# Performance work log

Hardware: AMD Instinct MI355X
Metric: run time of the kernel (lower is better)

## Reference

```python
import jax, jax.numpy as jnp
import numpy as np

TOP_K = 2

def setup_inputs() -> dict:
    key = jax.random.key(0)
    ks = jax.random.split(key, 8)
    B, S, H, E, F = 4, 2048, 1024, 8, 2048  # F = hidden * expansion(2)
    scale_in = 0.02
    return {
        "x": jax.random.normal(ks[0], (B, S, H), dtype=jnp.float32),
        "router_w": jax.random.normal(ks[1], (H, E), dtype=jnp.float32) * scale_in,
        "router_b": jnp.zeros((E,), dtype=jnp.float32),
        "w1": jax.random.normal(ks[2], (E, H, F), dtype=jnp.float32) * scale_in,
        "b1": jnp.zeros((E, F), dtype=jnp.float32),
        "w2": jax.random.normal(ks[3], (E, F, H), dtype=jnp.float32) * scale_in,
        "b2": jnp.zeros((E, H), dtype=jnp.float32),
    }

def reference(x, router_w, router_b, w1, b1, w2, b2):
    B, S, H = x.shape
    E = router_b.shape[0]
    T = B * S
    flat = x.reshape(T, H)
    # Router + top-k gating (softmax over the k selected logits, as in torch code)
    logits = flat @ router_w + router_b                       # [T, E]
    topk_scores, topk_idx = jax.lax.top_k(logits, TOP_K)      # [T, k]
    probs = jax.nn.softmax(topk_scores, axis=-1)              # [T, k]
    # Dense gate matrix: gates[t, e] = prob if e selected for token t else 0
    gates = jnp.zeros((T, E), dtype=flat.dtype).at[
        jnp.arange(T)[:, None], topk_idx
    ].add(probs)                                              # [T, E]
    # Expert FFNs computed as batched GEMMs over the expert axis
    h = jax.nn.relu(jnp.einsum('td,edf->etf', flat, w1) + b1[:, None, :])  # [E, T, F]
    eout = jnp.einsum('etf,efd->etd', h, w2) + b2[:, None, :]              # [E, T, H]
    out = jnp.einsum('etd,te->td', eout, gates)                            # [T, H]
    return out.reshape(B, S, H)
```

## Files before the change

### kernel.cpp

```cpp
#include <hip/hip_runtime.h>
#include <hip/hip_bf16.h>

#define T_TOK 8192
#define HDIM 1024
#define FDIM 2048
#define NEXP 8
#define NASSIGN (T_TOK * 2)
#define ROWCAP (NASSIGN + 128)
#define NHB 64

typedef __bf16 bf16;
typedef __bf16 bf16x4 __attribute__((ext_vector_type(4)));
typedef __bf16 bf16x8 __attribute__((ext_vector_type(8)));
typedef float f32x4 __attribute__((ext_vector_type(4)));

__device__ __forceinline__ void gload_lds16(const void* g, void* l) {
    __builtin_amdgcn_global_load_lds(
        (const __attribute__((address_space(1))) void*)(uintptr_t)g,
        (__attribute__((address_space(3))) void*)(uintptr_t)l,
        16, 0, 0);
}

__global__ __launch_bounds__(256) void transpose_to_bf16(
    const float* __restrict__ in, bf16* __restrict__ out, int R, int C) {
    __shared__ float tile[64][68];
    int e = blockIdx.z;
    const float* inp = in + (size_t)e * R * C;
    bf16* outp = out + (size_t)e * R * C;
    int c0 = blockIdx.x * 64, r0 = blockIdx.y * 64;
    int tid = threadIdx.x;
    int tx = tid & 15, ty = tid >> 4;
#pragma unroll
    for (int i = 0; i < 4; i++) {
        int row = ty + i * 16;
        float4 v = *(const float4*)&inp[(size_t)(r0 + row) * C + c0 + tx * 4];
        *(float4*)&tile[row][tx * 4] = v;
    }
    __syncthreads();
#pragma unroll
    for (int i = 0; i < 2; i++) {
        int idx = tid + i * 256;
        int c = idx >> 3, seg = idx & 7;
        bf16x8 v;
#pragma unroll
        for (int j = 0; j < 8; j++) v[j] = (bf16)tile[seg * 8 + j][c];
        *(bf16x8*)&outp[(size_t)(c0 + c) * R + r0 + seg * 8] = v;
    }
}

__global__ __launch_bounds__(256) void router_kernel(
    const float* __restrict__ x, const float* __restrict__ rw,
    const float* __restrict__ rb, int* __restrict__ expert_pair,
    float2* __restrict__ gate_pair) {
    __shared__ float rwT[NEXP][HDIM];
    __shared__ float rbs[NEXP];
    int tid = threadIdx.x;
    for (int i = tid; i < HDIM * NEXP / 4; i += 256) {
        float4 v = ((const float4*)rw)[i];
        int h = i >> 1, e0 = (i & 1) * 4;
        rwT[e0 + 0][h] = v.x;
        rwT[e0 + 1][h] = v.y;
        rwT[e0 + 2][h] = v.z;
        rwT[e0 + 3][h] = v.w;
    }
    if (tid < NEXP) rbs[tid] = rb[tid];
    __syncthreads();
    int wave = tid >> 6, lane = tid & 63;
    int tbase = blockIdx.x * 32 + wave * 8;

    for (int tk = 0; tk < 8; tk++) {
        int t = tbase + tk;
        const float4* xt = (const float4*)(x + (size_t)t * HDIM);
        float p[NEXP];
#pragma unroll
        for (int e = 0; e < NEXP; e++) p[e] = 0.f;
#pragma unroll
        for (int it = 0; it < 4; it++) {
            float4 v = xt[it * 64 + lane];
            int h = (it * 64 + lane) * 4;
#pragma unroll
            for (int e = 0; e < NEXP; e++) {
                float4 wv = *(const float4*)&rwT[e][h];
                p[e] += v.x * wv.x + v.y * wv.y + v.z * wv.z + v.w * wv.w;
            }
        }
#pragma unroll
        for (int off = 32; off >= 1; off >>= 1) {
#pragma unroll
            for (int e = 0; e < NEXP; e++) p[e] += __shfl_xor(p[e], off, 64);
        }
        if (lane == 0) {
            float lg[NEXP];
#pragma unroll
            for (int e = 0; e < NEXP; e++) lg[e] = p[e] + rbs[e];
            int e0 = 0;
#pragma unroll
            for (int e = 1; e < NEXP; e++)
                if (lg[e] > lg[e0]) e0 = e;
            int e1 = -1;
#pragma unroll
            for (int e = 0; e < NEXP; e++) {
                if (e == e0) continue;
                if (e1 < 0 || lg[e] > lg[e1]) e1 = e;
            }
            float z = expf(lg[e1] - lg[e0]);
            expert_pair[t] = e0 | (e1 << 16);
            gate_pair[t] = make_float2(1.f / (1.f + z), z / (1.f + z));
        }
    }
}

__global__ __launch_bounds__(256) void hist_kernel(
    const int* __restrict__ expert_pair, int* __restrict__ hist) {
    int tid = threadIdx.x;
    int wave = tid >> 6, lane = tid & 63;
    int a = blockIdx.x * 256 + tid;
    int t = a >> 1, j = a & 1;
    int e = (expert_pair[t] >> (16 * j)) & 0xffff;
    __shared__ int wcnt[4][NEXP];
#pragma unroll
    for (int ee = 0; ee < NEXP; ee++) {
        unsigned long long m = __ballot(e == ee);
        if (lane == 0) wcnt[wave][ee] = __popcll(m);
    }
    __syncthreads();
    if (tid < NEXP)
        hist[blockIdx.x * NEXP + tid] =
            wcnt[0][tid] + wcnt[1][tid] + wcnt[2][tid] + wcnt[3][tid];
}

__global__ __launch_bounds__(256) void scan_kernel(
    const int* __restrict__ hist, int* __restrict__ start,
    int* __restrict__ cnt, int* __restrict__ offs) {
    __shared__ int h[NHB * NEXP];
    __shared__ int tot[NEXP];
    __shared__ int offsh[NEXP];
    int tid = threadIdx.x;
    for (int i = tid; i < NHB * NEXP; i += 256) h[i] = hist[i];
    __syncthreads();
    if (tid < NEXP) {
        int s = 0;
        for (int b = 0; b < NHB; b++) s += h[b * NEXP + tid];
        tot[tid] = s;
        cnt[tid] = s;
    }
    __syncthreads();
    if (tid == 0) {
        int o = 0;
        for (int e = 0; e < NEXP; e++) {
            offsh[e] = o;
            offs[e] = o;
            o += tot[e];
        }
    }
    __syncthreads();
    if (tid < NEXP) {
        int run = offsh[tid];
        for (int b = 0; b < NHB; b++) {
            start[b * NEXP + tid] = run;
            run += h[b * NEXP + tid];
        }
    }
}

__global__ __launch_bounds__(256) void scatter_kernel(
    const int* __restrict__ expert_pair, const float2* __restrict__ gate_pair,
    const int* __restrict__ start, int* __restrict__ perm,
    float* __restrict__ gatebuf, int* __restrict__ rowbuf) {
    int tid = threadIdx.x;
    int wave = tid >> 6, lane = tid & 63;
    int a = blockIdx.x * 256 + tid;
    int t = a >> 1, j = a & 1;
    int e = (expert_pair[t] >> (16 * j)) & 0xffff;
    float2 gp = gate_pair[t];
    float g = j ? gp.y : gp.x;
    __shared__ int wcnt[4][NEXP];
    int rankw = 0;
    unsigned long long below = (1ull << lane) - 1ull;
#pragma unroll
    for (int ee = 0; ee < NEXP; ee++) {
        unsigned long long m = __ballot(e == ee);
        if (lane == 0) wcnt[wave][ee] = __popcll(m);
        if (ee == e) rankw = __popcll(m & below);
    }
    __syncthreads();
    int cross = 0;
    for (int w = 0; w < wave; w++) cross += wcnt[w][e];
    int pos = start[blockIdx.x * NEXP + e] + cross + rankw;
    perm[pos] = t;
    gatebuf[pos] = g;
    rowbuf[a] = pos;
}

__global__ __launch_bounds__(256) void pack_kernel(
    const float* __restrict__ x, const int* __restrict__ perm,
    bf16* __restrict__ xg) {
    int r0 = blockIdx.x * 16;
    int wave = threadIdx.x >> 6, lane = threadIdx.x & 63;
#pragma unroll
    for (int i = 0; i < 4; i++) {
        int row = r0 + wave * 4 + i;
        int tok = perm[row];
        const float* src = x + (size_t)tok * HDIM;
        bf16* dst = xg + (size_t)row * HDIM;
#pragma unroll
        for (int it = 0; it < 4; it++) {
            int c = (it * 64 + lane) * 4;
            float4 v = *(const float4*)&src[c];
            bf16x4 b = {(bf16)v.x, (bf16)v.y, (bf16)v.z, (bf16)v.w};
            *(bf16x4*)&dst[c] = b;
        }
    }
}

template <bool RELU, bool GATE>
__global__ __launch_bounds__(256) void moe_gemm(
    const bf16* __restrict__ A, const bf16* __restrict__ B,
    const float* __restrict__ bias, const float* __restrict__ gates,
    bf16* __restrict__ out, const int* __restrict__ cnt,
    const int* __restrict__ offs, int K, int N) {
    int e = blockIdx.z;
    int n_cnt = cnt[e];
    int m0 = blockIdx.y * 128;
    if (m0 >= n_cnt) return;
    int n0 = blockIdx.x * 128;

    __shared__ bf16 As[128 * 32];
    __shared__ bf16 Bs[128 * 32];

    int tid = threadIdx.x;
    int lane = tid & 63;
    int wave = tid >> 6;
    int wm = (wave & 1) * 64, wn = (wave >> 1) * 64;
    int quad = lane >> 4;
    int l16 = lane & 15;

    int off_e = offs[e];
    const bf16* Ae = A + (size_t)off_e * K;
    const bf16* Be = B + (size_t)e * N * K;

    int srow = lane >> 2;
    int scol = (lane & 3) ^ ((lane >> 2) & 3) ^ ((lane >> 4) & 3);
    const bf16* ag0 = Ae + (size_t)(m0 + wave * 16 + srow) * K + scol * 8;
    const bf16* ag1 = ag0 + (size_t)64 * K;
    const bf16* bg0 = Be + (size_t)(n0 + wave * 16 + srow) * K + scol * 8;
    const bf16* bg1 = bg0 + (size_t)64 * K;
    bf16* as0 = &As[(wave * 16) * 32];
    bf16* as1 = &As[(64 + wave * 16) * 32];
    bf16* bs0 = &Bs[(wave * 16) * 32];
    bf16* bs1 = &Bs[(64 + wave * 16) * 32];

    int dswz = (quad ^ (l16 & 3) ^ ((l16 >> 2) & 3)) * 8;

    f32x4 acc[4][4];
#pragma unroll
    for (int i = 0; i < 4; i++)
#pragma unroll
        for (int j = 0; j < 4; j++) acc[i][j] = f32x4{0.f, 0.f, 0.f, 0.f};

    for (int k0 = 0; k0 < K; k0 += 32) {
        gload_lds16(ag0 + k0, as0);
        gload_lds16(ag1 + k0, as1);
        gload_lds16(bg0 + k0, bs0);
        gload_lds16(bg1 + k0, bs1);
        __syncthreads();
        bf16x8 af[4], bfr[4];
#pragma unroll
        for (int i = 0; i < 4; i++)
            af[i] = *(const bf16x8*)&As[(wm + i * 16 + l16) * 32 + dswz];
#pragma unroll
        for (int j = 0; j < 4; j++)
            bfr[j] = *(const bf16x8*)&Bs[(wn + j * 16 + l16) * 32 + dswz];
#pragma unroll
        for (int i = 0; i < 4; i++)
#pragma unroll
            for (int j = 0; j < 4; j++)
                acc[i][j] = __builtin_amdgcn_mfma_f32_16x16x32_bf16(af[i], bfr[j], acc[i][j], 0, 0, 0);
        __syncthreads();
    }

#pragma unroll
    for (int i = 0; i < 4; i++)
#pragma unroll
        for (int j = 0; j < 4; j++)
#pragma unroll
            for (int r = 0; r < 4; r++) {
                int m = m0 + wm + i * 16 + quad * 4 + r;
                if (m < n_cnt) {
                    int n = n0 + wn + j * 16 + l16;
                    float v = acc[i][j][r] + bias[e * N + n];
                    if (RELU) v = v > 0.f ? v : 0.f;
                    if (GATE) v *= gates[off_e + m];
                    out[(size_t)(off_e + m) * N + n] = (bf16)v;
                }
            }
}

__global__ __launch_bounds__(256) void combine_kernel(
    const bf16* __restrict__ eout, const int* __restrict__ rowbuf,
    float* __restrict__ out) {
    int t = blockIdx.x;
    int r0 = rowbuf[2 * t], r1 = rowbuf[2 * t + 1];
    const bf16* p0 = eout + (size_t)r0 * HDIM;
    const bf16* p1 = eout + (size_t)r1 * HDIM;
    float* o = out + (size_t)t * HDIM;
    int n = threadIdx.x * 4;
    bf16x4 a = *(const bf16x4*)&p0[n];
    bf16x4 b = *(const bf16x4*)&p1[n];
    float4 v = {(float)a[0] + (float)b[0], (float)a[1] + (float)b[1],
                (float)a[2] + (float)b[2], (float)a[3] + (float)b[3]};
    *(float4*)&o[n] = v;
}

extern "C" void kernel_launch(void* const* d_in, const int* in_sizes, int n_in,
                              void* d_out, int out_size, void* d_ws, size_t ws_size,
                              hipStream_t stream) {
    const float* x = (const float*)d_in[0];
    const float* rw = (const float*)d_in[1];
    const float* rb = (const float*)d_in[2];
    const float* w1 = (const float*)d_in[3];
    const float* b1 = (const float*)d_in[4];
    const float* w2 = (const float*)d_in[5];
    const float* b2 = (const float*)d_in[6];
    float* out = (float*)d_out;

    char* ws = (char*)d_ws;
    size_t o = 0;
    auto alloc = [&](size_t bytes) {
        char* p = ws + o;
        o += (bytes + 255) & ~(size_t)255;
        return p;
    };
    bf16* w1t = (bf16*)alloc((size_t)NEXP * FDIM * HDIM * 2);
    bf16* w2t = (bf16*)alloc((size_t)NEXP * HDIM * FDIM * 2);
    bf16* hbuf = (bf16*)alloc((size_t)ROWCAP * FDIM * 2);
    bf16* xg = (bf16*)alloc((size_t)ROWCAP * HDIM * 2);
    bf16* eout = xg;
    int* expert_pair = (int*)alloc((size_t)T_TOK * 4);
    float2* gate_pair = (float2*)alloc((size_t)T_TOK * 8);
    int* hist = (int*)alloc((size_t)NHB * NEXP * 4);
    int* start = (int*)alloc((size_t)NHB * NEXP * 4);
    int* perm = (int*)alloc((size_t)NASSIGN * 4);
    float* gatebuf = (float*)alloc((size_t)NASSIGN * 4);
    int* rowbuf = (int*)alloc((size_t)NASSIGN * 4);
    int* cnt = (int*)alloc(256);
    int* offs = (int*)alloc(256);

    transpose_to_bf16<<<dim3(FDIM / 64, HDIM / 64, NEXP), 256, 0, stream>>>(w1, w1t, HDIM, FDIM);
    transpose_to_bf16<<<dim3(HDIM / 64, FDIM / 64, NEXP), 256, 0, stream>>>(w2, w2t, FDIM, HDIM);
    router_kernel<<<T_TOK / 32, 256, 0, stream>>>(x, rw, rb, expert_pair, gate_pair);
    hist_kernel<<<NHB, 256, 0, stream>>>(expert_pair, hist);
    scan_kernel<<<1, 256, 0, stream>>>(hist, start, cnt, offs);
    scatter_kernel<<<NHB, 256, 0, stream>>>(expert_pair, gate_pair, start, perm, gatebuf, rowbuf);
    pack_kernel<<<NASSIGN / 16, 256, 0, stream>>>(x, perm, xg);
    moe_gemm<true, false><<<dim3(FDIM / 128, T_TOK / 128, NEXP), 256, 0, stream>>>(
        xg, w1t, b1, nullptr, hbuf, cnt, offs, HDIM, FDIM);
    moe_gemm<false, true><<<dim3(HDIM / 128, T_TOK / 128, NEXP), 256, 0, stream>>>(
        hbuf, w2t, b2, gatebuf, eout, cnt, offs, FDIM, HDIM);
    combine_kernel<<<T_TOK, 256, 0, stream>>>(eout, rowbuf, out);
}
```

Measured before the change: 514.3 us.

## Double-buffer LDS tiles with BK=64 in MoE grouped GEMM

The grouped expert GEMM now uses a K-tile of 64 instead of 32 and keeps two LDS buffers. The next tile is prefetched with direct global-to-LDS loads while MFMAs run on the current one, which halves the barrier count per K and hides load latency. It also switches to a new XOR swizzle for the 64-wide rows, sets launch bounds to two blocks per CU, and grows the row capacity padding. LDS use per block rises to 64 KB, which may limit occupancy.

```diff
diff --git a/kernel.cpp b/kernel.cpp
--- a/kernel.cpp
+++ b/kernel.cpp
@@ -6,7 +6,7 @@
 #define FDIM 2048
 #define NEXP 8
 #define NASSIGN (T_TOK * 2)
-#define ROWCAP (NASSIGN + 128)
+#define ROWCAP (NASSIGN + 256)
 #define NHB 64
 
 typedef __bf16 bf16;
@@ -214,7 +214,7 @@
 }
 
 template <bool RELU, bool GATE>
-__global__ __launch_bounds__(256) void moe_gemm(
+__global__ __launch_bounds__(256, 2) void moe_gemm(
     const bf16* __restrict__ A, const bf16* __restrict__ B,
     const float* __restrict__ bias, const float* __restrict__ gates,
     bf16* __restrict__ out, const int* __restrict__ cnt,
@@ -225,8 +225,8 @@
     if (m0 >= n_cnt) return;
     int n0 = blockIdx.x * 128;
 
-    __shared__ bf16 As[128 * 32];
-    __shared__ bf16 Bs[128 * 32];
+    __shared__ bf16 As[2 * 128 * 64];
+    __shared__ bf16 Bs[2 * 128 * 64];
 
     int tid = threadIdx.x;
     int lane = tid & 63;
@@ -239,18 +239,12 @@
     const bf16* Ae = A + (size_t)off_e * K;
     const bf16* Be = B + (size_t)e * N * K;
 
-    int srow = lane >> 2;
-    int scol = (lane & 3) ^ ((lane >> 2) & 3) ^ ((lane >> 4) & 3);
-    const bf16* ag0 = Ae + (size_t)(m0 + wave * 16 + srow) * K + scol * 8;
-    const bf16* ag1 = ag0 + (size_t)64 * K;
-    const bf16* bg0 = Be + (size_t)(n0 + wave * 16 + srow) * K + scol * 8;
-    const bf16* bg1 = bg0 + (size_t)64 * K;
-    bf16* as0 = &As[(wave * 16) * 32];
-    bf16* as1 = &As[(64 + wave * 16) * 32];
-    bf16* bs0 = &Bs[(wave * 16) * 32];
-    bf16* bs1 = &Bs[(64 + wave * 16) * 32];
-
-    int dswz = (quad ^ (l16 & 3) ^ ((l16 >> 2) & 3)) * 8;
+    int srow = lane >> 3;
+    int sseg = (lane & 7) ^ srow;
+    const bf16* ag = Ae + (size_t)(m0 + wave * 8 + srow) * K + sseg * 8;
+    const bf16* bg = Be + (size_t)(n0 + wave * 8 + srow) * K + sseg * 8;
+    bf16* al = As + wave * 8 * 64;
+    bf16* bl = Bs + wave * 8 * 64;
 
     f32x4 acc[4][4];
 #pragma unroll
@@ -258,24 +252,48 @@
 #pragma unroll
         for (int j = 0; j < 4; j++) acc[i][j] = f32x4{0.f, 0.f, 0.f, 0.f};
 
-    for (int k0 = 0; k0 < K; k0 += 32) {
-        gload_lds16(ag0 + k0, as0);
-        gload_lds16(ag1 + k0, as1);
-        gload_lds16(bg0 + k0, bs0);
-        gload_lds16(bg1 + k0, bs1);
-        __syncthreads();
-        bf16x8 af[4], bfr[4];
-#pragma unroll
-        for (int i = 0; i < 4; i++)
-            af[i] = *(const bf16x8*)&As[(wm + i * 16 + l16) * 32 + dswz];
-#pragma unroll
-        for (int j = 0; j < 4; j++)
-            bfr[j] = *(const bf16x8*)&Bs[(wn + j * 16 + l16) * 32 + dswz];
-#pragma unroll
-        for (int i = 0; i < 4; i++)
+    int nk = K >> 6;
+
+#pragma unroll
+    for (int i = 0; i < 4; i++) {
+        gload_lds16(ag + (size_t)(i * 32) * K, al + i * 32 * 64);
+        gload_lds16(bg + (size_t)(i * 32) * K, bl + i * 32 * 64);
+    }
+    __syncthreads();
+
+    int swz = l16 & 7;
+    for (int kt = 0; kt < nk; kt++) {
+        int cur = kt & 1;
+        if (kt + 1 < nk) {
+            const bf16* ag2 = ag + (size_t)(kt + 1) * 64;
+            const bf16* bg2 = bg + (size_t)(kt + 1) * 64;
+            bf16* al2 = al + (cur ^ 1) * (128 * 64);
+            bf16* bl2 = bl + (cur ^ 1) * (128 * 64);
+#pragma unroll
+            for (int i = 0; i < 4; i++) {
+                gload_lds16(ag2 + (size_t)(i * 32) * K, al2 + i * 32 * 64);
+                gload_lds16(bg2 + (size_t)(i * 32) * K, bl2 + i * 32 * 64);
+            }
+        }
+        const bf16* ac = As + cur * (128 * 64);
+        const bf16* bc = Bs + cur * (128 * 64);
+#pragma unroll
+        for (int kk = 0; kk < 2; kk++) {
+            int sg = ((kk * 4 + quad) ^ swz) * 8;
+            bf16x8 af[4], bfr[4];
+#pragma unroll
+            for (int i = 0; i < 4; i++)
+                af[i] = *(const bf16x8*)&ac[(wm + i * 16 + l16) * 64 + sg];
 #pragma unroll
             for (int j = 0; j < 4; j++)
-                acc[i][j] = __builtin_amdgcn_mfma_f32_16x16x32_bf16(af[i], bfr[j], acc[i][j], 0, 0, 0);
+                bfr[j] = *(const bf16x8*)&bc[(wn + j * 16 + l16) * 64 + sg];
+#pragma unroll
+            for (int i = 0; i < 4; i++)
+#pragma unroll
+                for (int j = 0; j < 4; j++)
+                    acc[i][j] = __builtin_amdgcn_mfma_f32_16x16x32_bf16(
+                        af[i], bfr[j], acc[i][j], 0, 0, 0);
+        }
         __syncthreads();
     }
 
```

Result: faster. 488.8 us (-5.0%).

## Rewrite grouped MoE GEMM with 256x128 tiles, triple-buffered LDS, compact tile list

Applied to the files above, without the earlier changes.

The scan kernel now builds a compact list of (expert, m-tile) pairs at 256-row granularity, and the GEMM launches a 1D grid over only those active tiles. Block IDs are remapped so neighbouring tiles land on the same XCD. The GEMM uses 512 threads, a 256x128 block tile and a three-stage LDS ring filled by async global-to-LDS loads with explicit vmcnt waits, plus s_setprio around the MFMA bursts. This is meant to cut launch waste on empty tiles, reuse B across more rows and hide memory latency, at the cost of more LDS per block and extra padding rows per expert.

```diff
diff --git a/kernel.cpp b/kernel.cpp
--- a/kernel.cpp
+++ b/kernel.cpp
@@ -6,8 +6,10 @@
 #define FDIM 2048
 #define NEXP 8
 #define NASSIGN (T_TOK * 2)
-#define ROWCAP (NASSIGN + 128)
+#define ROWCAP (NASSIGN + 256)
 #define NHB 64
+#define MAXT 136
+#define MAXT2 72
 
 typedef __bf16 bf16;
 typedef __bf16 bf16x4 __attribute__((ext_vector_type(4)));
@@ -131,7 +133,9 @@
 
 __global__ __launch_bounds__(256) void scan_kernel(
     const int* __restrict__ hist, int* __restrict__ start,
-    int* __restrict__ cnt, int* __restrict__ offs) {
+    int* __restrict__ cnt, int* __restrict__ offs,
+    int* __restrict__ tile_e2, int* __restrict__ tile_m2,
+    int* __restrict__ ntiles2) {
     __shared__ int h[NHB * NEXP];
     __shared__ int tot[NEXP];
     __shared__ int offsh[NEXP];
@@ -152,6 +156,16 @@
             offs[e] = o;
             o += tot[e];
         }
+        int idx2 = 0;
+        for (int e = 0; e < NEXP; e++) {
+            int nt = (tot[e] + 255) >> 8;
+            for (int m = 0; m < nt; m++) {
+                tile_e2[idx2] = e;
+                tile_m2[idx2] = m;
+                idx2++;
+            }
+        }
+        ntiles2[0] = idx2;
     }
     __syncthreads();
     if (tid < NEXP) {
@@ -213,82 +227,122 @@
     }
 }
 
-template <bool RELU, bool GATE>
-__global__ __launch_bounds__(256) void moe_gemm(
+template <bool RELU, bool GATE, int K, int N>
+__global__ __launch_bounds__(512, 4) void moe_gemm_p(
     const bf16* __restrict__ A, const bf16* __restrict__ B,
     const float* __restrict__ bias, const float* __restrict__ gates,
     bf16* __restrict__ out, const int* __restrict__ cnt,
-    const int* __restrict__ offs, int K, int N) {
-    int e = blockIdx.z;
+    const int* __restrict__ offs, const int* __restrict__ tile_e2,
+    const int* __restrict__ tile_m2, const int* __restrict__ ntiles2) {
+    constexpr int NT = N / 128;
+    constexpr int nk = K / 32;
+    int ntl = ntiles2[0];
+    int nact = ntl * NT;
+    int f = blockIdx.x;
+    if (f >= nact) return;
+    int q8 = nact >> 3, r8 = nact & 7;
+    int xcd = f & 7, rest = f >> 3;
+    int wg = (xcd < r8) ? (xcd * (q8 + 1) + rest)
+                        : (r8 * (q8 + 1) + (xcd - r8) * q8 + rest);
+    int tile = wg / NT, ncol = wg - tile * NT;
+    int e = tile_e2[tile];
     int n_cnt = cnt[e];
-    int m0 = blockIdx.y * 128;
-    if (m0 >= n_cnt) return;
-    int n0 = blockIdx.x * 128;
-
-    __shared__ bf16 As[128 * 32];
-    __shared__ bf16 Bs[128 * 32];
+    int off_e = offs[e];
+    int m0 = tile_m2[tile] * 256;
+    int n0 = ncol * 128;
+
+    __shared__ bf16 As[3][256][32];
+    __shared__ bf16 Bs[3][128][32];
 
     int tid = threadIdx.x;
     int lane = tid & 63;
     int wave = tid >> 6;
-    int wm = (wave & 1) * 64, wn = (wave >> 1) * 64;
-    int quad = lane >> 4;
-    int l16 = lane & 15;
-
-    int off_e = offs[e];
+    int wm = wave & 1;
+    int wn = wave >> 1;
+    int quad = lane >> 4, l16 = lane & 15;
+    int rsw = (quad ^ ((l16 >> 1) & 3)) * 8;
+
     const bf16* Ae = A + (size_t)off_e * K;
-    const bf16* Be = B + (size_t)e * N * K;
-
-    int srow = lane >> 2;
-    int scol = (lane & 3) ^ ((lane >> 2) & 3) ^ ((lane >> 4) & 3);
-    const bf16* ag0 = Ae + (size_t)(m0 + wave * 16 + srow) * K + scol * 8;
-    const bf16* ag1 = ag0 + (size_t)64 * K;
-    const bf16* bg0 = Be + (size_t)(n0 + wave * 16 + srow) * K + scol * 8;
-    const bf16* bg1 = bg0 + (size_t)64 * K;
-    bf16* as0 = &As[(wave * 16) * 32];
-    bf16* as1 = &As[(64 + wave * 16) * 32];
-    bf16* bs0 = &Bs[(wave * 16) * 32];
-    bf16* bs1 = &Bs[(64 + wave * 16) * 32];
-
-    int dswz = (quad ^ (l16 & 3) ^ ((l16 >> 2) & 3)) * 8;
-
-    f32x4 acc[4][4];
-#pragma unroll
-    for (int i = 0; i < 4; i++)
-#pragma unroll
-        for (int j = 0; j < 4; j++) acc[i][j] = f32x4{0.f, 0.f, 0.f, 0.f};
-
-    for (int k0 = 0; k0 < K; k0 += 32) {
-        gload_lds16(ag0 + k0, as0);
-        gload_lds16(ag1 + k0, as1);
-        gload_lds16(bg0 + k0, bs0);
-        gload_lds16(bg1 + k0, bs1);
-        __syncthreads();
-        bf16x8 af[4], bfr[4];
-#pragma unroll
-        for (int i = 0; i < 4; i++)
-            af[i] = *(const bf16x8*)&As[(wm + i * 16 + l16) * 32 + dswz];
-#pragma unroll
-        for (int j = 0; j < 4; j++)
-            bfr[j] = *(const bf16x8*)&Bs[(wn + j * 16 + l16) * 32 + dswz];
-#pragma unroll
-        for (int i = 0; i < 4; i++)
-#pragma unroll
-            for (int j = 0; j < 4; j++)
-                acc[i][j] = __builtin_amdgcn_mfma_f32_16x16x32_bf16(af[i], bfr[j], acc[i][j], 0, 0, 0);
-        __syncthreads();
-    }
-
-#pragma unroll
-    for (int i = 0; i < 4; i++)
-#pragma unroll
-        for (int j = 0; j < 4; j++)
+    const bf16* Be = B + (size_t)e * (size_t)N * K;
+
+    int r0s = tid >> 2;
+    int segs = (tid & 3) ^ ((tid >> 3) & 3);
+    const bf16* agA0 = Ae + (size_t)(m0 + r0s) * K + segs * 8;
+    const bf16* agA1 = Ae + (size_t)(m0 + 128 + r0s) * K + segs * 8;
+    const bf16* bgB0 = Be + (size_t)(n0 + r0s) * K + segs * 8;
+
+    auto STG = [&](int buf, int kt) {
+        bf16* Ab = (bf16*)As + (size_t)buf * (256 * 32);
+        bf16* Bb = (bf16*)Bs + (size_t)buf * (128 * 32);
+        gload_lds16(agA0 + (size_t)kt * 32, Ab + (wave * 64) * 8);
+        gload_lds16(agA1 + (size_t)kt * 32, Ab + (512 + wave * 64) * 8);
+        gload_lds16(bgB0 + (size_t)kt * 32, Bb + (wave * 64) * 8);
+    };
+
+    f32x4 acc[8][2];
+#pragma unroll
+    for (int i = 0; i < 8; i++)
+#pragma unroll
+        for (int j = 0; j < 2; j++) acc[i][j] = f32x4{0.f, 0.f, 0.f, 0.f};
+
+    STG(0, 0);
+    STG(1, 1);
+
+    int b = 0, bs = 2;
+    for (int t = 0; t < nk; t++) {
+        if (t + 2 < nk) {
+            STG(bs, t + 2);
+            asm volatile("s_waitcnt vmcnt(6)" ::: "memory");
+        } else if (t + 2 == nk) {
+            asm volatile("s_waitcnt vmcnt(3)" ::: "memory");
+        } else {
+            asm volatile("s_waitcnt vmcnt(0)" ::: "memory");
+        }
+        asm volatile("s_barrier" ::: "memory");
+
+        const bf16* Ab = (const bf16*)As + (size_t)b * (256 * 32);
+        const bf16* Bb = (const bf16*)Bs + (size_t)b * (128 * 32);
+        bf16x8 bf0 = *(const bf16x8*)(Bb + (wn * 32 + 0 * 16 + l16) * 32 + rsw);
+        bf16x8 bf1 = *(const bf16x8*)(Bb + (wn * 32 + 1 * 16 + l16) * 32 + rsw);
+        bf16x8 af[4];
+#pragma unroll
+        for (int mi = 0; mi < 4; mi++)
+            af[mi] = *(const bf16x8*)(Ab + (wm * 128 + mi * 16 + l16) * 32 + rsw);
+        asm volatile("s_waitcnt lgkmcnt(0)" ::: "memory");
+        __builtin_amdgcn_s_setprio(1);
+#pragma unroll
+        for (int mi = 0; mi < 4; mi++) {
+            acc[mi][0] = __builtin_amdgcn_mfma_f32_16x16x32_bf16(af[mi], bf0, acc[mi][0], 0, 0, 0);
+            acc[mi][1] = __builtin_amdgcn_mfma_f32_16x16x32_bf16(af[mi], bf1, acc[mi][1], 0, 0, 0);
+        }
+        __builtin_amdgcn_s_setprio(0);
+#pragma unroll
+        for (int mi = 0; mi < 4; mi++)
+            af[mi] = *(const bf16x8*)(Ab + (wm * 128 + (4 + mi) * 16 + l16) * 32 + rsw);
+        asm volatile("s_waitcnt lgkmcnt(0)" ::: "memory");
+        __builtin_amdgcn_s_setprio(1);
+#pragma unroll
+        for (int mi = 0; mi < 4; mi++) {
+            acc[4 + mi][0] = __builtin_amdgcn_mfma_f32_16x16x32_bf16(af[mi], bf0, acc[4 + mi][0], 0, 0, 0);
+            acc[4 + mi][1] = __builtin_amdgcn_mfma_f32_16x16x32_bf16(af[mi], bf1, acc[4 + mi][1], 0, 0, 0);
+        }
+        __builtin_amdgcn_s_setprio(0);
+        asm volatile("s_barrier" ::: "memory");
+
+        b = (b == 2) ? 0 : b + 1;
+        bs = (bs == 2) ? 0 : bs + 1;
+    }
+
+#pragma unroll
+    for (int mi = 0; mi < 8; mi++)
+#pragma unroll
+        for (int nj = 0; nj < 2; nj++)
 #pragma unroll
             for (int r = 0; r < 4; r++) {
-                int m = m0 + wm + i * 16 + quad * 4 + r;
+                int m = m0 + wm * 128 + mi * 16 + quad * 4 + r;
                 if (m < n_cnt) {
-                    int n = n0 + wn + j * 16 + l16;
-                    float v = acc[i][j][r] + bias[e * N + n];
+                    int n = n0 + wn * 32 + nj * 16 + l16;
+                    float v = acc[mi][nj][r] + bias[e * N + n];
                     if (RELU) v = v > 0.f ? v : 0.f;
                     if (GATE) v *= gates[off_e + m];
                     out[(size_t)(off_e + m) * N + n] = (bf16)v;
@@ -345,17 +399,20 @@
     int* rowbuf = (int*)alloc((size_t)NASSIGN * 4);
     int* cnt = (int*)alloc(256);
     int* offs = (int*)alloc(256);
+    int* tile_e2 = (int*)alloc((size_t)MAXT2 * 4);
+    int* tile_m2 = (int*)alloc((size_t)MAXT2 * 4);
+    int* ntiles2 = (int*)alloc(256);
 
     transpose_to_bf16<<<dim3(FDIM / 64, HDIM / 64, NEXP), 256, 0, stream>>>(w1, w1t, HDIM, FDIM);
     transpose_to_bf16<<<dim3(HDIM / 64, FDIM / 64, NEXP), 256, 0, stream>>>(w2, w2t, FDIM, HDIM);
     router_kernel<<<T_TOK / 32, 256, 0, stream>>>(x, rw, rb, expert_pair, gate_pair);
     hist_kernel<<<NHB, 256, 0, stream>>>(expert_pair, hist);
-    scan_kernel<<<1, 256, 0, stream>>>(hist, start, cnt, offs);
+    scan_kernel<<<1, 256, 0, stream>>>(hist, start, cnt, offs, tile_e2, tile_m2, ntiles2);
     scatter_kernel<<<NHB, 256, 0, stream>>>(expert_pair, gate_pair, start, perm, gatebuf, rowbuf);
     pack_kernel<<<NASSIGN / 16, 256, 0, stream>>>(x, perm, xg);
-    moe_gemm<true, false><<<dim3(FDIM / 128, T_TOK / 128, NEXP), 256, 0, stream>>>(
-        xg, w1t, b1, nullptr, hbuf, cnt, offs, HDIM, FDIM);
-    moe_gemm<false, true><<<dim3(HDIM / 128, T_TOK / 128, NEXP), 256, 0, stream>>>(
-        hbuf, w2t, b2, gatebuf, eout, cnt, offs, FDIM, HDIM);
+    moe_gemm_p<true, false, HDIM, FDIM><<<dim3(MAXT2 * (FDIM / 128)), 512, 0, stream>>>(
+        xg, w1t, b1, nullptr, hbuf, cnt, offs, tile_e2, tile_m2, ntiles2);
+    moe_gemm_p<false, true, FDIM, HDIM><<<dim3(MAXT2 * (HDIM / 128)), 512, 0, stream>>>(
+        hbuf, w2t, b2, gatebuf, eout, cnt, offs, tile_e2, tile_m2, ntiles2);
     combine_kernel<<<T_TOK, 256, 0, stream>>>(eout, rowbuf, out);
 }
```

After: 458.8 us. 10.8% less time.
